# Kernel tuning notes

Hardware: AMD Instinct MI355X
Metric: run time of the kernel (lower is better)

## Reference

```python
import jax, jax.numpy as jnp
import numpy as np

HEADS = 16
DIM_HEAD = 64
SCALE = DIM_HEAD ** -0.5


def setup_inputs() -> dict:
    key = jax.random.key(0)
    k1, k2, k3, k4 = jax.random.split(key, 4)
    dim = 1024
    inner = HEADS * DIM_HEAD  # 1024
    b, n = 4, 2048
    x = jax.random.normal(k1, (b, n, dim), dtype=jnp.float32)
    # weights stored as [in, out] (equivalent math to torch Linear)
    w_qkv = jax.random.normal(k2, (dim, inner * 3), dtype=jnp.float32) * (dim ** -0.5)
    w_out = jax.random.normal(k3, (inner, dim), dtype=jnp.float32) * (inner ** -0.5)
    b_out = jax.random.normal(k4, (dim,), dtype=jnp.float32) * 0.01
    return {"x": x, "w_qkv": w_qkv, "w_out": w_out, "b_out": b_out}


def reference(x, w_qkv, w_out, b_out):
    b, n, dim = x.shape
    qkv = x @ w_qkv                                   # [b, n, 3*inner]
    q, k, v = jnp.split(qkv, 3, axis=-1)
    def to_heads(t):
        return t.reshape(b, n, HEADS, DIM_HEAD).transpose(0, 2, 1, 3)  # b h n d
    q, k, v = to_heads(q) * SCALE, to_heads(k), to_heads(v)
    dots = jnp.einsum('bhid,bhjd->bhij', q, k)        # [b, h, n, n]
    mask_value = -jnp.finfo(dots.dtype).max
    causal_mask = jnp.triu(jnp.ones((n, n), dtype=bool), k=1)
    dots = jnp.where(causal_mask, mask_value, dots)
    attn = jax.nn.softmax(dots, axis=-1)
    out = jnp.einsum('bhij,bhjd->bhid', attn, v)      # [b, h, n, d]
    out = out.transpose(0, 2, 1, 3).reshape(b, n, HEADS * DIM_HEAD)
    return out @ w_out + b_out
```

## Files before the change

kernel.cpp:

```cpp
#include <hip/hip_runtime.h>
#include <hip/hip_bf16.h>
#include <stdint.h>

typedef __attribute__((ext_vector_type(8))) short bf16x8;
typedef __attribute__((ext_vector_type(4))) float f32x4;
typedef __attribute__((ext_vector_type(4))) unsigned int uint32x4;

#define TOKENS 8192
#define DMODEL 1024
#define NQKV   3072
#define NSEQ   2048
#define NHEAD  16
#define DHEAD  64


__device__ __forceinline__ ushort f32_bf16(float f) {
    uint32_t u = __builtin_bit_cast(uint32_t, f);
    u = (u + 0x7fffu + ((u >> 16) & 1u)) >> 16;
    return (ushort)u;
}

__device__ __forceinline__ unsigned int cvt_pk_bf16(float lo, float hi) {
    unsigned int r;
    asm("v_cvt_pk_bf16_f32 %0, %1, %2" : "=v"(r) : "v"(lo), "v"(hi));
    return r;
}
__device__ __forceinline__ void permlane32_swap(unsigned int& a, unsigned int& b) {
    asm("v_permlane32_swap_b32 %0, %1" : "+v"(a), "+v"(b));
}
__device__ __forceinline__ void permlane16_swap(unsigned int& a, unsigned int& b) {
    asm("v_permlane16_swap_b32 %0, %1" : "+v"(a), "+v"(b));
}
__device__ __forceinline__ unsigned opaque_copy(unsigned x) {
    unsigned y;
    asm("v_mov_b32 %0, %1" : "=v"(y) : "v"(x));
    return y;
}

__device__ __forceinline__ float red_max_g(float x) {
    unsigned a = __builtin_bit_cast(unsigned, x);
    unsigned b = opaque_copy(a);
    permlane16_swap(a, b);
    float r = fmaxf(__builtin_bit_cast(float, a), __builtin_bit_cast(float, b));
    unsigned c = __builtin_bit_cast(unsigned, r);
    unsigned d = opaque_copy(c);
    permlane32_swap(c, d);
    return fmaxf(__builtin_bit_cast(float, c), __builtin_bit_cast(float, d));
}
__device__ __forceinline__ float red_sum_g(float x) {
    unsigned a = __builtin_bit_cast(unsigned, x);
    unsigned b = opaque_copy(a);
    permlane16_swap(a, b);
    float r = __builtin_bit_cast(float, a) + __builtin_bit_cast(float, b);
    unsigned c = __builtin_bit_cast(unsigned, r);
    unsigned d = opaque_copy(c);
    permlane32_swap(c, d);
    return __builtin_bit_cast(float, c) + __builtin_bit_cast(float, d);
}

__device__ __forceinline__ void gload16(const void* g, void* l) {
    __builtin_amdgcn_global_load_lds(
        (const __attribute__((address_space(1))) void*)g,
        (__attribute__((address_space(3))) void*)l, 16, 0, 0);
}

__global__ void cvt_x_kernel(const float* __restrict__ x, ushort* __restrict__ xb) {
    int i = blockIdx.x * 256 + threadIdx.x;
    float4 v = reinterpret_cast<const float4*>(x)[i];
    ushort4 o;
    o.x = f32_bf16(v.x); o.y = f32_bf16(v.y);
    o.z = f32_bf16(v.z); o.w = f32_bf16(v.w);
    reinterpret_cast<ushort4*>(xb)[i] = o;
}

__global__ __launch_bounds__(256) void cvt_wt_kernel(
    const float* __restrict__ w, ushort* __restrict__ wt, int N)
{
    __shared__ float tile[64][65];
    const int tid = threadIdx.x;
    const int r  = tid >> 4;
    const int c4 = (tid & 15) * 4;
    const int n0 = blockIdx.x * 64;
    const int k0 = blockIdx.y * 64;
    #pragma unroll
    for (int i = 0; i < 4; ++i) {
        const float4 v = *reinterpret_cast<const float4*>(&w[(size_t)(k0 + r + i * 16) * N + n0 + c4]);
        tile[r + i * 16][c4 + 0] = v.x;
        tile[r + i * 16][c4 + 1] = v.y;
        tile[r + i * 16][c4 + 2] = v.z;
        tile[r + i * 16][c4 + 3] = v.w;
    }
    __syncthreads();
    #pragma unroll
    for (int i = 0; i < 4; ++i) {
        ushort4 o;
        o.x = f32_bf16(tile[c4 + 0][r + i * 16]);
        o.y = f32_bf16(tile[c4 + 1][r + i * 16]);
        o.z = f32_bf16(tile[c4 + 2][r + i * 16]);
        o.w = f32_bf16(tile[c4 + 3][r + i * 16]);
        *reinterpret_cast<ushort4*>(&wt[(size_t)(n0 + r + i * 16) * 1024 + k0 + c4]) = o;
    }
}

template<int MODE>
__global__ __launch_bounds__(256) void gemm_bt(
    const ushort* __restrict__ A, const ushort* __restrict__ Bt,
    ushort* __restrict__ Qb, ushort* __restrict__ Kb, ushort* __restrict__ Vtb,
    float* __restrict__ Out, const float* __restrict__ bias)
{
    constexpr int K = 1024;
    __shared__ __align__(16) ushort As[128 * 32];
    __shared__ __align__(16) ushort Bs[128 * 32];

    const int lane = threadIdx.x & 63;
    const int w    = threadIdx.x >> 6;
    const int l16  = lane & 15;
    const int g    = lane >> 4;
    const int row0 = blockIdx.y * 128;
    const int col0 = blockIdx.x * 128;
    const int wr   = (w >> 1) * 64;
    const int wc   = (w & 1) * 64;

    const int srow  = w * 16 + (lane >> 2);
    const int sswz8 = ((lane & 3) ^ ((lane >> 3) & 3)) * 8;
    const ushort* Ag = A  + (size_t)(row0 + srow) * K + sswz8;
    const ushort* Bg = Bt + (size_t)(col0 + srow) * K + sswz8;
    ushort* AsW = As + w * (16 * 32);
    ushort* BsW = Bs + w * (16 * 32);

    const int cq8 = (g ^ ((l16 >> 1) & 3)) * 8;

    f32x4 acc[4][4] = {};

    for (int kk = 0; kk < K; kk += 32) {
        gload16(Ag + kk,          AsW);
        gload16(Ag + 64 * K + kk, AsW + 64 * 32);
        gload16(Bg + kk,          BsW);
        gload16(Bg + 64 * K + kk, BsW + 64 * 32);
        __syncthreads();
        bf16x8 a[4], b[4];
        #pragma unroll
        for (int m = 0; m < 4; ++m)
            a[m] = *reinterpret_cast<const bf16x8*>(&As[(wr + m * 16 + l16) * 32 + cq8]);
        #pragma unroll
        for (int n = 0; n < 4; ++n)
            b[n] = *reinterpret_cast<const bf16x8*>(&Bs[(wc + n * 16 + l16) * 32 + cq8]);
        #pragma unroll
        for (int m = 0; m < 4; ++m)
            #pragma unroll
            for (int n = 0; n < 4; ++n)
                acc[m][n] = __builtin_amdgcn_mfma_f32_16x16x32_bf16(a[m], b[n], acc[m][n], 0, 0, 0);
        __syncthreads();
    }

    if (MODE == 0) {
        const int part = col0 >> 10;
        const float QSC = 0.18033688011112042f;
        #pragma unroll
        for (int m = 0; m < 4; ++m) {
            const int trow = row0 + wr + m * 16 + 4 * g;
            #pragma unroll
            for (int n = 0; n < 4; ++n) {
                const int c  = col0 + wc + n * 16 + l16;
                const int cc = c & 1023;
                const int h  = cc >> 6, d = cc & 63;
                #pragma unroll
                for (int jj = 0; jj < 4; ++jj) {
                    const int t  = trow + jj;
                    const int bb = t >> 11, nn = t & 2047;
                    const float v = acc[m][n][jj];
                    const size_t bhid = (size_t)(bb * NHEAD + h);
                    if (part == 0)
                        Qb[(bhid * NSEQ + nn) * DHEAD + d] = f32_bf16(v * QSC);
                    else if (part == 1)
                        Kb[(bhid * NSEQ + nn) * DHEAD + d] = f32_bf16(v);
                    else
                        Vtb[bhid * (NSEQ * DHEAD) + (size_t)(nn >> 5) * (DHEAD * 32)
                            + d * 32 + (nn & 31)] = f32_bf16(v);
                }
            }
        }
    } else {
        #pragma unroll
        for (int m = 0; m < 4; ++m) {
            const int trow = row0 + wr + m * 16 + 4 * g;
            #pragma unroll
            for (int n = 0; n < 4; ++n) {
                const int c = col0 + wc + n * 16 + l16;
                const float bv = bias[c];
                #pragma unroll
                for (int jj = 0; jj < 4; ++jj)
                    Out[(size_t)(trow + jj) * DMODEL + c] = acc[m][n][jj] + bv;
            }
        }
    }
}

__device__ __forceinline__ void attn_qk(
    int kt, int qr0s, int l16, int g,
    const bf16x8 (&kk)[4][2],
    const bf16x8 qf0, const bf16x8 qf1,
    f32x4 (&oacc)[4], float& mrun, float& lsum,
    bf16x8& pf0, bf16x8& pf1)
{
    const f32x4 zero = {};
    f32x4 s[4];
    __builtin_amdgcn_s_setprio(1);
    #pragma unroll
    for (int t = 0; t < 4; ++t) {
        s[t] = __builtin_amdgcn_mfma_f32_16x16x32_bf16(kk[t][0], qf0, zero, 0, 0, 0);
        s[t] = __builtin_amdgcn_mfma_f32_16x16x32_bf16(kk[t][1], qf1, s[t], 0, 0, 0);
    }
    __builtin_amdgcn_s_setprio(0);
    if (kt + 63 > qr0s) {
        const int kb = kt + 4 * g - (qr0s + l16);
        #pragma unroll
        for (int t = 0; t < 4; ++t)
            #pragma unroll
            for (int jj = 0; jj < 4; ++jj)
                if (kb + 16 * t + jj > 0) s[t][jj] = -1e30f;
    }
    const float m0 = fmaxf(fmaxf(s[0][0], s[0][1]), s[0][2]);
    const float m1 = fmaxf(fmaxf(s[0][3], s[1][0]), s[1][1]);
    const float m2 = fmaxf(fmaxf(s[1][2], s[1][3]), s[2][0]);
    const float m3 = fmaxf(fmaxf(s[2][1], s[2][2]), s[2][3]);
    const float m4 = fmaxf(fmaxf(s[3][0], s[3][1]), s[3][2]);
    const float m5 = fmaxf(fmaxf(m0, m1), m2);
    const float m6 = fmaxf(fmaxf(m3, m4), s[3][3]);
    float mx = red_max_g(fmaxf(m5, m6));
    if (__any(mx > mrun + 8.0f)) {
        const float mn = fmaxf(mrun, mx);
        const float sc = __builtin_amdgcn_exp2f(mrun - mn);
        mrun = mn;
        lsum *= sc;
        float scj[4];
        #pragma unroll
        for (int jj = 0; jj < 4; ++jj) scj[jj] = __shfl(sc, 4 * g + jj);
        #pragma unroll
        for (int dt = 0; dt < 4; ++dt)
            #pragma unroll
            for (int jj = 0; jj < 4; ++jj) oacc[dt][jj] *= scj[jj];
    }
    float ps = 0.f;
    unsigned int pw[4][2];
    #pragma unroll
    for (int t = 0; t < 4; ++t) {
        const float p0 = __builtin_amdgcn_exp2f(s[t][0] - mrun);
        const float p1 = __builtin_amdgcn_exp2f(s[t][1] - mrun);
        const float p2 = __builtin_amdgcn_exp2f(s[t][2] - mrun);
        const float p3 = __builtin_amdgcn_exp2f(s[t][3] - mrun);
        ps += (p0 + p1) + (p2 + p3);
        pw[t][0] = cvt_pk_bf16(p0, p1);
        pw[t][1] = cvt_pk_bf16(p2, p3);
    }
    lsum += red_sum_g(ps);
    unsigned int a0 = pw[0][0], a1 = pw[0][1], b0 = pw[1][0], b1 = pw[1][1];
    permlane32_swap(a0, b0); permlane32_swap(a1, b1);
    permlane16_swap(a0, b0); permlane16_swap(a1, b1);
    pf0 = __builtin_bit_cast(bf16x8, (uint32x4){a0, a1, b0, b1});
    unsigned int c0 = pw[2][0], c1 = pw[2][1], d0 = pw[3][0], d1 = pw[3][1];
    permlane32_swap(c0, d0); permlane32_swap(c1, d1);
    permlane16_swap(c0, d0); permlane16_swap(c1, d1);
    pf1 = __builtin_bit_cast(bf16x8, (uint32x4){c0, c1, d0, d1});
}

__global__ __launch_bounds__(256) void attn_kernel(
    const ushort* __restrict__ Qb, const ushort* __restrict__ Kb,
    const ushort* __restrict__ Vt, ushort* __restrict__ Ob)
{
    __shared__ __align__(16) ushort Klds[2][4096];
    __shared__ __align__(16) ushort Vlds[2][4096];

    const int lane = threadIdx.x & 63;
    const int w    = threadIdx.x >> 6;
    const int l16  = lane & 15;
    const int g    = lane >> 4;

    const int bid = blockIdx.x;
    const int xcd = bid & 7, ii = bid >> 3;
    const int bh  = xcd * 8 + (ii >> 4);
    const int jlo = ii & 15;
    const int jhi = 31 - jlo;

    const int qr0_lo = jlo * 64 + w * 16;
    const int qr0_hi = jhi * 64 + w * 16;
    const int nt = jhi + 1;

    const ushort* QpL = Qb + ((size_t)bh * NSEQ + qr0_lo + l16) * DHEAD + 8 * g;
    const ushort* QpH = Qb + ((size_t)bh * NSEQ + qr0_hi + l16) * DHEAD + 8 * g;
    const bf16x8 qfL0 = *reinterpret_cast<const bf16x8*>(QpL);
    const bf16x8 qfL1 = *reinterpret_cast<const bf16x8*>(QpL + 32);
    const bf16x8 qfH0 = *reinterpret_cast<const bf16x8*>(QpH);
    const bf16x8 qfH1 = *reinterpret_cast<const bf16x8*>(QpH + 32);

    const ushort* Kg = Kb + (size_t)bh * (NSEQ * DHEAD);
    const ushort* Vg = Vt + (size_t)bh * (NSEQ * DHEAD);

    const int q0    = w * 2;
    const int srow  = lane >> 2;
    const int sswz8 = ((lane & 3) ^ ((lane >> 3) & 3)) * 8;
    const int cq8   = (g ^ ((l16 >> 1) & 3)) * 8;

    f32x4 oaccL[4] = {}, oaccH[4] = {};
    float mrunL = -1e30f, lsumL = 0.f, mrunH = -1e30f, lsumH = 0.f;

    #pragma unroll
    for (int i = 0; i < 2; ++i) {
        const int q = q0 + i;
        gload16(Kg + (size_t)((q & 3) * 16 + srow) * 64 + (q >> 2) * 32 + sswz8,
                &Klds[0][q * 512]);
        gload16(Vg + (size_t)(q >> 2) * 2048 + ((q & 3) * 16 + srow) * 32 + sswz8,
                &Vlds[0][q * 512]);
    }
    __syncthreads();

    for (int t = 0; t < nt; ++t) {
        const int cur = t & 1;
        if (t + 1 < nt) {
            const int kt1 = (t + 1) * 64;
            #pragma unroll
            for (int i = 0; i < 2; ++i) {
                const int q = q0 + i;
                gload16(Kg + (size_t)(kt1 + (q & 3) * 16 + srow) * 64 + (q >> 2) * 32 + sswz8,
                        &Klds[cur ^ 1][q * 512]);
                gload16(Vg + (size_t)kt1 * 64 + (q >> 2) * 2048 + ((q & 3) * 16 + srow) * 32 + sswz8,
                        &Vlds[cur ^ 1][q * 512]);
            }
        }
        const int kt = t * 64;
        bf16x8 kk[4][2];
        #pragma unroll
        for (int tt = 0; tt < 4; ++tt) {
            #pragma unroll
            for (int h = 0; h < 2; ++h)
                kk[tt][h] = *reinterpret_cast<const bf16x8*>(
                    &Klds[cur][h * 2048 + (16 * tt + l16) * 32 + cq8]);
        }
        bf16x8 pfH0, pfH1, pfL0, pfL1;
        attn_qk(kt, qr0_hi, l16, g, kk, qfH0, qfH1, oaccH, mrunH, lsumH, pfH0, pfH1);
        const bool doLo = (t <= jlo);
        if (doLo)
            attn_qk(kt, qr0_lo, l16, g, kk, qfL0, qfL1, oaccL, mrunL, lsumL, pfL0, pfL1);
        __builtin_amdgcn_s_setprio(1);
        #pragma unroll
        for (int dt = 0; dt < 4; ++dt) {
            const bf16x8 v0 = *reinterpret_cast<const bf16x8*>(
                &Vlds[cur][(dt * 16 + l16) * 32 + cq8]);
            const bf16x8 v1 = *reinterpret_cast<const bf16x8*>(
                &Vlds[cur][2048 + (dt * 16 + l16) * 32 + cq8]);
            oaccH[dt] = __builtin_amdgcn_mfma_f32_16x16x32_bf16(pfH0, v0, oaccH[dt], 0, 0, 0);
            oaccH[dt] = __builtin_amdgcn_mfma_f32_16x16x32_bf16(pfH1, v1, oaccH[dt], 0, 0, 0);
            if (doLo) {
                oaccL[dt] = __builtin_amdgcn_mfma_f32_16x16x32_bf16(pfL0, v0, oaccL[dt], 0, 0, 0);
                oaccL[dt] = __builtin_amdgcn_mfma_f32_16x16x32_bf16(pfL1, v1, oaccL[dt], 0, 0, 0);
            }
        }
        __builtin_amdgcn_s_setprio(0);
        __syncthreads();
    }

    const int bb = bh >> 4, h = bh & 15;
    {
        const float inv = 1.0f / lsumH;
        float invj[4];
        #pragma unroll
        for (int jj = 0; jj < 4; ++jj) invj[jj] = __shfl(inv, 4 * g + jj);
        #pragma unroll
        for (int jj = 0; jj < 4; ++jj) {
            const size_t t = (size_t)bb * NSEQ + qr0_hi + 4 * g + jj;
            #pragma unroll
            for (int dt = 0; dt < 4; ++dt)
                Ob[t * DMODEL + h * DHEAD + dt * 16 + l16] = f32_bf16(oaccH[dt][jj] * invj[jj]);
        }
    }
    {
        const float inv = 1.0f / lsumL;
        float invj[4];
        #pragma unroll
        for (int jj = 0; jj < 4; ++jj) invj[jj] = __shfl(inv, 4 * g + jj);
        #pragma unroll
        for (int jj = 0; jj < 4; ++jj) {
            const size_t t = (size_t)bb * NSEQ + qr0_lo + 4 * g + jj;
            #pragma unroll
            for (int dt = 0; dt < 4; ++dt)
                Ob[t * DMODEL + h * DHEAD + dt * 16 + l16] = f32_bf16(oaccL[dt][jj] * invj[jj]);
        }
    }
}

extern "C" void kernel_launch(void* const* d_in, const int* in_sizes, int n_in,
                              void* d_out, int out_size, void* d_ws, size_t ws_size,
                              hipStream_t stream)
{
    const float* x     = (const float*)d_in[0];
    const float* w_qkv = (const float*)d_in[1];
    const float* w_out = (const float*)d_in[2];
    const float* b_out = (const float*)d_in[3];
    float* out = (float*)d_out;

    char* ws = (char*)d_ws;
    ushort* x_bf   = (ushort*)(ws);
    ushort* wqkv_t = (ushort*)(ws + 16777216);
    ushort* wout_t = (ushort*)(ws + 23068672);
    ushort* q_bf   = (ushort*)(ws + 25165824);
    ushort* k_bf   = (ushort*)(ws + 41943040);
    ushort* vt_bf  = (ushort*)(ws + 58720256);
    ushort* attn_bf = x_bf;

    cvt_x_kernel<<<dim3(TOKENS * DMODEL / 4 / 256), dim3(256), 0, stream>>>(x, x_bf);
    cvt_wt_kernel<<<dim3(NQKV / 64, 1024 / 64), dim3(256), 0, stream>>>(w_qkv, wqkv_t, NQKV);
    cvt_wt_kernel<<<dim3(1024 / 64, 1024 / 64), dim3(256), 0, stream>>>(w_out, wout_t, 1024);

    gemm_bt<0><<<dim3(NQKV / 128, TOKENS / 128), dim3(256), 0, stream>>>(
        x_bf, wqkv_t, q_bf, k_bf, vt_bf, nullptr, nullptr);

    attn_kernel<<<dim3(1024), dim3(256), 0, stream>>>(q_bf, k_bf, vt_bf, attn_bf);

    gemm_bt<1><<<dim3(DMODEL / 128, TOKENS / 128), dim3(256), 0, stream>>>(
        attn_bf, wout_t, nullptr, nullptr, nullptr, out, b_out);
}
```

Before: 214.9 us.

## Double-buffer LDS tiles in bf16 GEMM to overlap global loads with MFMA

The GEMM main loop now keeps two LDS buffers for the A and B tiles and unrolls by two K-steps. The next tile is issued as direct global-to-LDS loads while MFMAs consume the current buffer, which drops one barrier per step and hides load latency. LDS use per block doubles to 32KB, which may reduce occupancy. The overlap also depends on how gload16's wait counts interact with the barriers.

```diff
diff --git a/kernel.cpp b/kernel.cpp
--- a/kernel.cpp
+++ b/kernel.cpp
@@ -109,8 +109,8 @@
     float* __restrict__ Out, const float* __restrict__ bias)
 {
     constexpr int K = 1024;
-    __shared__ __align__(16) ushort As[128 * 32];
-    __shared__ __align__(16) ushort Bs[128 * 32];
+    __shared__ __align__(16) ushort As[2][128 * 32];
+    __shared__ __align__(16) ushort Bs[2][128 * 32];
 
     const int lane = threadIdx.x & 63;
     const int w    = threadIdx.x >> 6;
@@ -125,33 +125,49 @@
     const int sswz8 = ((lane & 3) ^ ((lane >> 3) & 3)) * 8;
     const ushort* Ag = A  + (size_t)(row0 + srow) * K + sswz8;
     const ushort* Bg = Bt + (size_t)(col0 + srow) * K + sswz8;
-    ushort* AsW = As + w * (16 * 32);
-    ushort* BsW = Bs + w * (16 * 32);
+    const int woff = w * (16 * 32);
 
     const int cq8 = (g ^ ((l16 >> 1) & 3)) * 8;
 
     f32x4 acc[4][4] = {};
 
-    for (int kk = 0; kk < K; kk += 32) {
-        gload16(Ag + kk,          AsW);
-        gload16(Ag + 64 * K + kk, AsW + 64 * 32);
-        gload16(Bg + kk,          BsW);
-        gload16(Bg + 64 * K + kk, BsW + 64 * 32);
+#define GSTAGE(BUF, KK) do {                                             \
+        gload16(Ag + (KK),          &As[BUF][woff]);                     \
+        gload16(Ag + 64 * K + (KK), &As[BUF][woff + 64 * 32]);           \
+        gload16(Bg + (KK),          &Bs[BUF][woff]);                     \
+        gload16(Bg + 64 * K + (KK), &Bs[BUF][woff + 64 * 32]);           \
+    } while (0)
+
+#define GCOMPUTE(BUF) do {                                               \
+        bf16x8 a[4], b[4];                                               \
+        _Pragma("unroll")                                                \
+        for (int m = 0; m < 4; ++m)                                      \
+            a[m] = *reinterpret_cast<const bf16x8*>(                     \
+                &As[BUF][(wr + m * 16 + l16) * 32 + cq8]);               \
+        _Pragma("unroll")                                                \
+        for (int n = 0; n < 4; ++n)                                      \
+            b[n] = *reinterpret_cast<const bf16x8*>(                     \
+                &Bs[BUF][(wc + n * 16 + l16) * 32 + cq8]);               \
+        _Pragma("unroll")                                                \
+        for (int m = 0; m < 4; ++m)                                      \
+            _Pragma("unroll")                                            \
+            for (int n = 0; n < 4; ++n)                                  \
+                acc[m][n] = __builtin_amdgcn_mfma_f32_16x16x32_bf16(     \
+                    a[m], b[n], acc[m][n], 0, 0, 0);                     \
+    } while (0)
+
+    GSTAGE(0, 0);
+    __syncthreads();
+    for (int kk = 0; kk < K; kk += 64) {
+        GSTAGE(1, kk + 32);
+        GCOMPUTE(0);
         __syncthreads();
-        bf16x8 a[4], b[4];
-        #pragma unroll
-        for (int m = 0; m < 4; ++m)
-            a[m] = *reinterpret_cast<const bf16x8*>(&As[(wr + m * 16 + l16) * 32 + cq8]);
-        #pragma unroll
-        for (int n = 0; n < 4; ++n)
-            b[n] = *reinterpret_cast<const bf16x8*>(&Bs[(wc + n * 16 + l16) * 32 + cq8]);
-        #pragma unroll
-        for (int m = 0; m < 4; ++m)
-            #pragma unroll
-            for (int n = 0; n < 4; ++n)
-                acc[m][n] = __builtin_amdgcn_mfma_f32_16x16x32_bf16(a[m], b[n], acc[m][n], 0, 0, 0);
+        if (kk + 64 < K) GSTAGE(0, kk + 64);
+        GCOMPUTE(1);
         __syncthreads();
     }
+#undef GSTAGE
+#undef GCOMPUTE
 
     if (MODE == 0) {
         const int part = col0 >> 10;
```

Result: slower. 219.3 us (+2.0%).

## Pipeline GEMM loads with 4-stage LDS ring and defer softmax reductions

Applied to the files above, without the earlier changes.

The GEMM main loop now uses a four-buffer LDS ring with async global-to-LDS loads issued three stages ahead. It waits with explicit vmcnt counts and a single barrier per iteration instead of two __syncthreads. In attention, the cross-lane row-max reduction only runs when some lane's local max exceeds the running max by the threshold. The row-sum reduction is deferred to the epilogue, removing permlane work from the inner loop. The cost is four times the GEMM LDS footprint, which may lower occupancy, plus correctness that depends on the hand-set waitcnt values and on deferring the sum being valid when lanes share the same running max.

```diff
diff --git a/kernel.cpp b/kernel.cpp
--- a/kernel.cpp
+++ b/kernel.cpp
@@ -12,7 +12,6 @@
 #define NSEQ   2048
 #define NHEAD  16
 #define DHEAD  64
-
 
 __device__ __forceinline__ ushort f32_bf16(float f) {
     uint32_t u = __builtin_bit_cast(uint32_t, f);
@@ -62,6 +61,12 @@
     __builtin_amdgcn_global_load_lds(
         (const __attribute__((address_space(1))) void*)g,
         (__attribute__((address_space(3))) void*)l, 16, 0, 0);
+}
+
+__device__ __forceinline__ void barf() {
+    asm volatile("" ::: "memory");
+    __builtin_amdgcn_s_barrier();
+    asm volatile("" ::: "memory");
 }
 
 __global__ void cvt_x_kernel(const float* __restrict__ x, ushort* __restrict__ xb) {
@@ -108,9 +113,10 @@
     ushort* __restrict__ Qb, ushort* __restrict__ Kb, ushort* __restrict__ Vtb,
     float* __restrict__ Out, const float* __restrict__ bias)
 {
-    constexpr int K = 1024;
-    __shared__ __align__(16) ushort As[128 * 32];
-    __shared__ __align__(16) ushort Bs[128 * 32];
+    constexpr int K  = 1024;
+    constexpr int NT = K / 32;
+    __shared__ __align__(16) ushort As[4][128 * 32];
+    __shared__ __align__(16) ushort Bs[4][128 * 32];
 
     const int lane = threadIdx.x & 63;
     const int w    = threadIdx.x >> 6;
@@ -125,33 +131,47 @@
     const int sswz8 = ((lane & 3) ^ ((lane >> 3) & 3)) * 8;
     const ushort* Ag = A  + (size_t)(row0 + srow) * K + sswz8;
     const ushort* Bg = Bt + (size_t)(col0 + srow) * K + sswz8;
-    ushort* AsW = As + w * (16 * 32);
-    ushort* BsW = Bs + w * (16 * 32);
+    const int woff = w * (16 * 32);
 
     const int cq8 = (g ^ ((l16 >> 1) & 3)) * 8;
 
     f32x4 acc[4][4] = {};
 
-    for (int kk = 0; kk < K; kk += 32) {
-        gload16(Ag + kk,          AsW);
-        gload16(Ag + 64 * K + kk, AsW + 64 * 32);
-        gload16(Bg + kk,          BsW);
-        gload16(Bg + 64 * K + kk, BsW + 64 * 32);
-        __syncthreads();
+#define GSTAGE(T) do { const int _b = (T) & 3; const int _k = (T) * 32;  \
+        gload16(Ag + _k,          &As[_b][woff]);                        \
+        gload16(Ag + 64 * K + _k, &As[_b][woff + 64 * 32]);              \
+        gload16(Bg + _k,          &Bs[_b][woff]);                        \
+        gload16(Bg + 64 * K + _k, &Bs[_b][woff + 64 * 32]);              \
+    } while (0)
+
+    GSTAGE(0); GSTAGE(1); GSTAGE(2);
+
+    for (int t = 0; t < NT; ++t) {
+        if (t < NT - 2)       asm volatile("s_waitcnt vmcnt(8)" ::: "memory");
+        else if (t == NT - 2) asm volatile("s_waitcnt vmcnt(4)" ::: "memory");
+        else                  asm volatile("s_waitcnt vmcnt(0)" ::: "memory");
+        barf();
+        const int buf = t & 3;
         bf16x8 a[4], b[4];
         #pragma unroll
         for (int m = 0; m < 4; ++m)
-            a[m] = *reinterpret_cast<const bf16x8*>(&As[(wr + m * 16 + l16) * 32 + cq8]);
+            a[m] = *reinterpret_cast<const bf16x8*>(
+                &As[buf][(wr + m * 16 + l16) * 32 + cq8]);
         #pragma unroll
         for (int n = 0; n < 4; ++n)
-            b[n] = *reinterpret_cast<const bf16x8*>(&Bs[(wc + n * 16 + l16) * 32 + cq8]);
+            b[n] = *reinterpret_cast<const bf16x8*>(
+                &Bs[buf][(wc + n * 16 + l16) * 32 + cq8]);
+        if (t + 3 < NT) GSTAGE(t + 3);
+        __builtin_amdgcn_s_setprio(1);
         #pragma unroll
         for (int m = 0; m < 4; ++m)
             #pragma unroll
             for (int n = 0; n < 4; ++n)
-                acc[m][n] = __builtin_amdgcn_mfma_f32_16x16x32_bf16(a[m], b[n], acc[m][n], 0, 0, 0);
-        __syncthreads();
-    }
+                acc[m][n] = __builtin_amdgcn_mfma_f32_16x16x32_bf16(
+                    a[m], b[n], acc[m][n], 0, 0, 0);
+        __builtin_amdgcn_s_setprio(0);
+    }
+#undef GSTAGE
 
     if (MODE == 0) {
         const int part = col0 >> 10;
@@ -227,8 +247,9 @@
     const float m4 = fmaxf(fmaxf(s[3][0], s[3][1]), s[3][2]);
     const float m5 = fmaxf(fmaxf(m0, m1), m2);
     const float m6 = fmaxf(fmaxf(m3, m4), s[3][3]);
-    float mx = red_max_g(fmaxf(m5, m6));
-    if (__any(mx > mrun + 8.0f)) {
+    const float mxl = fmaxf(m5, m6);
+    if (__any(mxl > mrun + 8.0f)) {
+        const float mx = red_max_g(mxl);
         const float mn = fmaxf(mrun, mx);
         const float sc = __builtin_amdgcn_exp2f(mrun - mn);
         mrun = mn;
@@ -253,7 +274,7 @@
         pw[t][0] = cvt_pk_bf16(p0, p1);
         pw[t][1] = cvt_pk_bf16(p2, p3);
     }
-    lsum += red_sum_g(ps);
+    lsum += ps;
     unsigned int a0 = pw[0][0], a1 = pw[0][1], b0 = pw[1][0], b1 = pw[1][1];
     permlane32_swap(a0, b0); permlane32_swap(a1, b1);
     permlane16_swap(a0, b0); permlane16_swap(a1, b1);
@@ -361,7 +382,7 @@
 
     const int bb = bh >> 4, h = bh & 15;
     {
-        const float inv = 1.0f / lsumH;
+        const float inv = 1.0f / red_sum_g(lsumH);
         float invj[4];
         #pragma unroll
         for (int jj = 0; jj < 4; ++jj) invj[jj] = __shfl(inv, 4 * g + jj);
@@ -374,7 +395,7 @@
         }
     }
     {
-        const float inv = 1.0f / lsumL;
+        const float inv = 1.0f / red_sum_g(lsumL);
         float invj[4];
         #pragma unroll
         for (int jj = 0; jj < 4; ++jj) invj[jj] = __shfl(inv, 4 * g + jj);
```

Result: no change. 212.7 us (-1.0%).
